# Performance work log

Hardware: AMD Instinct MI355X
Metric: run time of the kernel (lower is better)

The kernel has to match this reference:

```python
import jax, jax.numpy as jnp
import numpy as np

N, E, G = 50000, 400000, 64   # nodes, edges, graphs
HEADS = 4
F_IN, H1, C3, OUT = 64, 96, 64, 10  # in feats, hidden (3*32), last conv out, classes


def seg_softmax(alpha, index, num_segments):
    # numerically stable softmax over segments (PyG softmax(alpha, edge_index_i))
    amax = jax.ops.segment_max(alpha, index, num_segments)
    amax = jnp.where(jnp.isfinite(amax), amax, 0.0)
    e = jnp.exp(alpha - amax[index])
    denom = jax.ops.segment_sum(e, index, num_segments)
    return e / (denom[index] + 1e-16)


def general_conv(x, src, dst, Wm, bm, att, Ws=None, bs=None):
    # GeneralConv (attention=True, additive, directed_msg, aggr='add')
    C = att.shape[-1]
    m = (x[src] @ Wm + bm).reshape(-1, HEADS, C)              # [E,H,C] gathered messages
    a = jax.nn.leaky_relu((m * att).sum(-1), 0.2)             # [E,H] attention logits
    a = seg_softmax(a, dst, N)                                # segment softmax per dest node
    agg = jax.ops.segment_sum(m * a[..., None], dst, N)       # [N,H,C] scatter-add
    out = agg.mean(axis=1)                                    # head mean -> [N,C]
    if Ws is None:                                            # lin_self = Identity (in==out)
        return out + x
    return out + x @ Ws + bs


def setup_inputs():
    key = jax.random.key(0)
    ks = jax.random.split(key, 16)
    s = 0.05
    return {
        "x": jax.random.normal(ks[0], (N, F_IN), jnp.float32),
        "edge_index": jax.random.randint(ks[1], (2, E), 0, N, jnp.int32),
        "batch": jnp.sort(jax.random.randint(ks[2], (N,), 0, G, jnp.int32)),
        # layer 1: F_IN -> H1
        "Wm1": jax.random.normal(ks[3], (F_IN, HEADS * H1), jnp.float32) * s,
        "bm1": jnp.zeros((HEADS * H1,), jnp.float32),
        "att1": jax.random.normal(ks[4], (HEADS, H1), jnp.float32) * s,
        "Ws1": jax.random.normal(ks[5], (F_IN, H1), jnp.float32) * s,
        "bs1": jnp.zeros((H1,), jnp.float32),
        # layer 2: H1 -> H1 (lin_self = Identity)
        "Wm2": jax.random.normal(ks[6], (H1, HEADS * H1), jnp.float32) * s,
        "bm2": jnp.zeros((HEADS * H1,), jnp.float32),
        "att2": jax.random.normal(ks[7], (HEADS, H1), jnp.float32) * s,
        # layer 3: H1 -> C3
        "Wm3": jax.random.normal(ks[8], (H1, HEADS * C3), jnp.float32) * s,
        "bm3": jnp.zeros((HEADS * C3,), jnp.float32),
        "att3": jax.random.normal(ks[9], (HEADS, C3), jnp.float32) * s,
        "Ws3": jax.random.normal(ks[10], (H1, C3), jnp.float32) * s,
        "bs3": jnp.zeros((C3,), jnp.float32),
        # classifier
        "Wfc": jax.random.normal(ks[11], (C3, OUT), jnp.float32) * s,
        "bfc": jnp.zeros((OUT,), jnp.float32),
    }


def reference(x, edge_index, batch, Wm1, bm1, att1, Ws1, bs1,
              Wm2, bm2, att2, Wm3, bm3, att3, Ws3, bs3, Wfc, bfc):
    src, dst = edge_index[0], edge_index[1]
    h = general_conv(x, src, dst, Wm1, bm1, att1, Ws1, bs1)
    h = general_conv(h, src, dst, Wm2, bm2, att2)
    h = general_conv(h, src, dst, Wm3, bm3, att3, Ws3, bs3)
    # global_mean_pool
    ssum = jax.ops.segment_sum(h, batch, G)
    cnt = jax.ops.segment_sum(jnp.ones((N, 1), h.dtype), batch, G)
    pooled = ssum / jnp.maximum(cnt, 1.0)                      # [G,C3]
    logits = pooled @ Wfc + bfc
    return jax.nn.log_softmax(logits, axis=1)
```

## Files before the change

### kernel.cpp

```cpp
#include <hip/hip_runtime.h>
#include <hip/hip_bf16.h>
#include <stdint.h>

using bf16 = __hip_bfloat16;
typedef __attribute__((ext_vector_type(8))) short bf16x8;
typedef __attribute__((ext_vector_type(4))) float f32x4;
typedef __attribute__((ext_vector_type(2))) float f32x2;

#define NN 50000
#define NE 400000
#define NG 64
#define FIN 64
#define HID 96
#define CC3 64
#define NOUT 10

#define SCAN_BLOCK 256
#define NPART ((NN + SCAN_BLOCK - 1) / SCAN_BLOCK)

__device__ __forceinline__ float b2f(bf16 h){ return __bfloat162float(h); }
__device__ __forceinline__ bf16 f2b(float f){ return __float2bfloat16(f); }
__device__ __forceinline__ float blo(unsigned v){ return __uint_as_float(v << 16); }
__device__ __forceinline__ float bhi(unsigned v){ return __uint_as_float(v & 0xFFFF0000u); }

struct PrepA {
  const float *Wm1,*att1,*bm1,*Wm2,*att2,*bm2,*Wm3,*att3,*bm3,*bs1;
  float *f2,*f3,*lbv,*zb; bf16* WTf1;
  int* deg; float* psum; int* done;
};
__global__ __launch_bounds__(256) void prep_a_kernel(PrepA j){
  int bid = blockIdx.x;
  if (bid == 0){
    for (int i=threadIdx.x; i<96*4; i+=256){
      int k=i>>2, h=i&3; float a=0.f;
      for (int c=0;c<96;++c) a += j.Wm2[k*384 + h*96 + c]*j.att2[h*96+c];
      j.f2[i]=a;
    }
    for (int i=threadIdx.x; i<96*4; i+=256){
      int k=i>>2, h=i&3; float a=0.f;
      for (int c=0;c<64;++c) a += j.Wm3[k*256 + h*64 + c]*j.att3[h*64+c];
      j.f3[i]=a;
    }
    for (int i=threadIdx.x; i<16*64; i+=256){
      int col=i>>6, k=i&63; float a=0.f;
      if (col<4){ for (int c=0;c<96;++c) a += j.Wm1[k*384 + col*96 + c]*j.att1[col*96+c]; }
      j.WTf1[i] = f2b(a);
    }
    if (threadIdx.x < 96) j.zb[threadIdx.x] = 0.f;
    __syncthreads();
    if (threadIdx.x < 4){
      int h = threadIdx.x;
      float l1=0.f,l2=0.f,l3=0.f;
      for (int c=0;c<96;++c) l1 += j.bm1[h*96+c]*j.att1[h*96+c];
      for (int c=0;c<96;++c) l2 += j.bm2[h*96+c]*j.att2[h*96+c];
      for (int c=0;c<64;++c) l3 += j.bm3[h*64+c]*j.att3[h*64+c];
      float e2 = l2;
      for (int k=0;k<96;++k) e2 += j.bs1[k]*j.f2[k*4+h];
      j.lbv[h]=l1; j.lbv[4+h]=e2; j.lbv[8+h]=l3;
    }
  } else if (bid <= NPART){
    int i=(bid-1)*256+threadIdx.x;
    if (i<NN) j.deg[i]=0;
  } else {
    for (int i=threadIdx.x; i<NG*CC3; i+=256) j.psum[i]=0.f;
    if (threadIdx.x==0) *j.done = 0;
  }
}

struct PrepB {
  const float *Wm1,*bm1,*Ws1,*Wm2,*bm2,*Wm3,*bm3,*Ws3;
  const float *f2,*f3;
  bf16 *WT1,*WT2,*WT3;
};
__device__ __forceinline__ float w1full(const PrepB& j, int k, int c){
  if (k < 256) return 0.25f*j.Wm1[(k&63)*384 + (k>>6)*96 + c];
  if (k == 256) return 0.25f*(j.bm1[c]+j.bm1[96+c]+j.bm1[192+c]+j.bm1[288+c]);
  if (k < 288) return 0.f;
  return j.Ws1[(k-288)*96 + c];
}
__device__ __forceinline__ float w2full(const PrepB& j, int k, int c){
  if (k < 384){ int kk=k%96, h=k/96; return 0.25f*j.Wm2[kk*384 + h*96 + c]; }
  if (k == 384) return 0.25f*(j.bm2[c]+j.bm2[96+c]+j.bm2[192+c]+j.bm2[288+c]);
  if (k < 416) return 0.f;
  return (k-416==c) ? 1.f : 0.f;
}
__device__ __forceinline__ float w3full(const PrepB& j, int k, int c){
  if (k < 384){ int kk=k%96, h=k/96; return 0.25f*j.Wm3[kk*256 + h*64 + c]; }
  if (k == 384) return 0.25f*(j.bm3[c]+j.bm3[64+c]+j.bm3[128+c]+j.bm3[192+c]);
  if (k < 416) return 0.f;
  return j.Ws3[(k-416)*64 + c];
}
__global__ __launch_bounds__(256) void prep_b_kernel(PrepB j){
  int idx = blockIdx.x*256 + threadIdx.x;
  if (idx < 112*384){
    int col = idx/384, k = idx - col*384;
    float v;
    if (k >= 352) v = 0.f;
    else if (col < 96) v = w1full(j,k,col);
    else if (col < 100){ int h=col-96; float a=0.f;
      for (int c=0;c<96;++c) a += w1full(j,k,c)*j.f2[c*4+h]; v=a; }
    else v = 0.f;
    j.WT1[col*384 + k] = f2b(v);
  } else if (idx < 112*384 + 112*512){
    int r = idx - 112*384;
    int col = r/512, k = r - col*512;
    float v;
    if (col < 96) v = w2full(j,k,col);
    else if (col < 100){ int h=col-96; float a=0.f;
      for (int c=0;c<96;++c) a += w2full(j,k,c)*j.f3[c*4+h]; v=a; }
    else v = 0.f;
    j.WT2[col*512 + k] = f2b(v);
  } else {
    int r = idx - 112*384 - 112*512;
    int col = r/512, k = r - col*512;
    j.WT3[col*512 + k] = f2b(w3full(j,k,col));
  }
}

__global__ void deg_kernel(const int* __restrict__ ei, int* __restrict__ deg){
  int e = blockIdx.x*256 + threadIdx.x;
  if (e < NE) atomicAdd(&deg[ei[NE + e]], 1);
}

__global__ __launch_bounds__(256) void scan_part_kernel(const int* __restrict__ deg,
    int* __restrict__ partials, int* __restrict__ done, int* __restrict__ off){
  __shared__ int ws[4];
  __shared__ int lastflag;
  __shared__ int buf[256];
  int i = blockIdx.x*SCAN_BLOCK + threadIdx.x;
  int v = (i < NN) ? deg[i] : 0;
  int lane = threadIdx.x & 63, w = threadIdx.x >> 6;
  int s = v;
  #pragma unroll
  for (int m=1;m<64;m<<=1) s += __shfl_xor(s,m);
  if (lane==0) ws[w]=s;
  __syncthreads();
  if (threadIdx.x==0){
    int tot = ws[0]+ws[1]+ws[2]+ws[3];
    atomicExch(&partials[blockIdx.x], tot);
    __threadfence();
    int old = atomicAdd(done, 1);
    lastflag = (old == NPART-1) ? 1 : 0;
  }
  __syncthreads();
  if (lastflag){
    int t = threadIdx.x;
    int pv = (t < NPART) ? atomicAdd(&partials[t], 0) : 0;
    buf[t] = pv; __syncthreads();
    for (int st=1; st<256; st<<=1){
      int x = (t>=st) ? buf[t-st] : 0;
      __syncthreads();
      buf[t] += x;
      __syncthreads();
    }
    if (t < NPART) atomicExch(&partials[t], buf[t] - pv);
    if (t == 0) off[NN] = buf[255];
  }
}

__global__ __launch_bounds__(256) void scan_final_kernel(const int* __restrict__ deg,
    const int* __restrict__ partials, int* __restrict__ off, int* __restrict__ cursor){
  __shared__ int buf[256];
  int i = blockIdx.x*SCAN_BLOCK + threadIdx.x;
  int t = threadIdx.x;
  int v = (i<NN) ? deg[i] : 0;
  buf[t] = v; __syncthreads();
  for (int s=1;s<256;s<<=1){
    int x = (t>=s) ? buf[t-s] : 0;
    __syncthreads();
    buf[t] += x;
    __syncthreads();
  }
  int ex = partials[blockIdx.x] + buf[t] - v;
  if (i<NN){ off[i]=ex; cursor[i]=ex; }
}

__global__ void scatter_kernel(const int* __restrict__ ei, int* __restrict__ cursor,
                               int* __restrict__ csr_src){
  int e = blockIdx.x*256 + threadIdx.x;
  if (e < NE){
    int d = ei[NE + e];
    int slot = atomicAdd(&cursor[d], 1);
    csr_src[slot] = ei[e];
  }
}

__global__ __launch_bounds__(256) void el1_kernel(const float* __restrict__ x,
    const bf16* __restrict__ WTf1, const float* __restrict__ lbv,
    bf16* __restrict__ xb, uint8_t* __restrict__ x8, float* __restrict__ EL)
{
  const int wave = threadIdx.x>>6, lane = threadIdx.x&63;
  const int tile = blockIdx.x*4 + wave;
  if (tile >= NN/16) return;
  const int lm = lane&15, q = lane>>4;
  const size_t row = (size_t)tile*16 + lm;
  bf16x8 xf[2];
  #pragma unroll
  for (int kt=0;kt<2;++kt){
    float4 a0 = *(const float4*)(x + row*64 + kt*32 + q*8);
    float4 a1 = *(const float4*)(x + row*64 + kt*32 + q*8 + 4);
    bf16 t[8] = {f2b(a0.x),f2b(a0.y),f2b(a0.z),f2b(a0.w),
                 f2b(a1.x),f2b(a1.y),f2b(a1.z),f2b(a1.w)};
    xf[kt] = *(const bf16x8*)t;
    *(bf16x8*)(xb + row*64 + kt*32 + q*8) = xf[kt];
    int p0 = 0, p1 = 0;
    p0 = __builtin_amdgcn_cvt_pk_fp8_f32(a0.x, a0.y, p0, false);
    p0 = __builtin_amdgcn_cvt_pk_fp8_f32(a0.z, a0.w, p0, true);
    p1 = __builtin_amdgcn_cvt_pk_fp8_f32(a1.x, a1.y, p1, false);
    p1 = __builtin_amdgcn_cvt_pk_fp8_f32(a1.z, a1.w, p1, true);
    uint2 pk; pk.x = (unsigned)p0; pk.y = (unsigned)p1;
    *(uint2*)(x8 + row*64 + kt*32 + q*8) = pk;
  }
  f32x4 acc = {};
  #pragma unroll
  for (int kt=0;kt<2;++kt){
    bf16x8 wf = *(const bf16x8*)(WTf1 + (size_t)lm*64 + kt*32 + q*8);
    acc = __builtin_amdgcn_mfma_f32_16x16x32_bf16(wf, xf[kt], acc, 0,0,0);
  }
  if (q==0){
    float4 e; float l;
    l=acc[0]+lbv[0]; l=(l>=0.f)?l:0.2f*l; e.x=__expf(fminf(fmaxf(l,-60.f),60.f));
    l=acc[1]+lbv[1]; l=(l>=0.f)?l:0.2f*l; e.y=__expf(fminf(fmaxf(l,-60.f),60.f));
    l=acc[2]+lbv[2]; l=(l>=0.f)?l:0.2f*l; e.z=__expf(fminf(fmaxf(l,-60.f),60.f));
    l=acc[3]+lbv[3]; l=(l>=0.f)?l:0.2f*l; e.w=__expf(fminf(fmaxf(l,-60.f),60.f));
    *(float4*)(EL + 4*row) = e;
  }
}

template<int KH>
__global__ __launch_bounds__(256) void agg_kernel(
    const int* __restrict__ off, const int* __restrict__ csr_src,
    const float* __restrict__ ELin, const uint8_t* __restrict__ T8,
    bf16* __restrict__ Sb)
{
  constexpr int R  = 4*KH;
  constexpr int KS = R + 32;
  const int wave = threadIdx.x >> 6, lane = threadIdx.x & 63;
  const int n = blockIdx.x*4 + wave;
  const int e0 = off[n], e1 = off[n+1];

  const bool act = (8*lane) < R;
  const int hidx = min(3, (8*lane)/KH);
  const int kk = (8*lane) % KH;

  float acc[8] = {0.f,0.f,0.f,0.f,0.f,0.f,0.f,0.f};
  float dnl = 0.f;

  for (int base=e0; base<e1; base+=8){
    const int cnt = min(8, e1-base);
    int sreg = (lane < cnt) ? csr_src[base+lane] : 0;
    int sv[8];
    #pragma unroll
    for (int j=0;j<8;++j) sv[j] = __shfl(sreg, j);
    float wl[8]; uint2 u[8];
    #pragma unroll
    for (int j=0;j<8;++j){
      wl[j] = ELin[4*(size_t)sv[j] + hidx];
      u[j]  = *(const uint2*)(T8 + (size_t)sv[j]*KH + kk);
    }
    #pragma unroll
    for (int j=0;j<8;++j){
      float w = (j < cnt) ? wl[j] : 0.f;
      dnl += w;
      f32x2 a0 = __builtin_amdgcn_cvt_pk_f32_fp8((int)u[j].x, false);
      f32x2 a1 = __builtin_amdgcn_cvt_pk_f32_fp8((int)u[j].x, true);
      f32x2 a2 = __builtin_amdgcn_cvt_pk_f32_fp8((int)u[j].y, false);
      f32x2 a3 = __builtin_amdgcn_cvt_pk_f32_fp8((int)u[j].y, true);
      acc[0] += a0.x*w;  acc[1] += a0.y*w;
      acc[2] += a1.x*w;  acc[3] += a1.y*w;
      acc[4] += a2.x*w;  acc[5] += a2.y*w;
      acc[6] += a3.x*w;  acc[7] += a3.y*w;
    }
  }

  const float rd = 1.f/(dnl + 1e-16f);
  bf16* srow = Sb + (size_t)n*KS;
  if (act){
    bf16 st[8];
    #pragma unroll
    for (int t=0;t<8;++t) st[t] = f2b(acc[t]*rd);
    *(bf16x8*)(srow + 8*lane) = *(const bf16x8*)st;
  } else if (8*lane < KS){
    bf16 st[8] = {};
    if (8*lane == R) st[0] = f2b((e1 > e0) ? 1.f : 0.f);
    *(bf16x8*)(srow + 8*lane) = *(const bf16x8*)st;
  }
}

template<int KH, int NCT, bool POOL>
__global__ __launch_bounds__(256, 4) void gemm_kernel(
    const bf16* __restrict__ Sb, const bf16* __restrict__ Hprev,
    const bf16* __restrict__ WT, const float* __restrict__ bias,
    const float* __restrict__ lbe, bf16* __restrict__ Hout,
    uint8_t* __restrict__ H8out, float* __restrict__ ELout,
    const int* __restrict__ batch, float* __restrict__ psum)
{
  constexpr int R      = 4*KH;
  constexpr int KS     = R + 32;
  constexpr int KA     = KS + KH;
  constexpr int KTS    = KS/32;
  constexpr int NKT    = KA/32;
  constexpr int NCHUNK = (NKT + 3)/4;
  constexpr int KAP    = NCHUNK*128;
  constexpr int NCOL   = NCT*16;
  constexpr int NT     = NN/16;
  constexpr int WSZ    = NCOL*256;
  constexpr int OSZ    = POOL ? (4*16*68*4) : (4*16*104*2);
  constexpr int USZ    = (WSZ > OSZ) ? WSZ : OSZ;
  __shared__ __align__(16) unsigned char lds[USZ];

  const int tid  = threadIdx.x;
  const int wave = tid >> 6, lane = tid & 63;
  const int lm = lane & 15, q = lane >> 4;
  const int tile = blockIdx.x*4 + wave;
  const bool active = (tile < NT);
  const size_t row = (size_t)tile*16 + lm;

  const bf16* arow = Sb + row*KS;
  const bf16* hrow = Hprev + row*KH;
  const unsigned sw = (unsigned)((lm & 7) << 4);

  f32x4 acc[NCT];
  #pragma unroll
  for (int c=0;c<NCT;++c) acc[c] = (f32x4){0.f,0.f,0.f,0.f};

  #pragma unroll
  for (int chunk=0; chunk<NCHUNK; ++chunk){
    if (chunk) __syncthreads();
    {
      const int k0 = chunk*128;
      for (int idx = tid; idx < NCOL*16; idx += 256){
        const int col = idx >> 4, sg = idx & 15;
        uint4 v = *(const uint4*)(WT + (size_t)col*KAP + k0 + sg*8);
        const unsigned off = (unsigned)(sg*16) ^ (unsigned)((col & 7) << 4);
        *(uint4*)(lds + col*256 + off) = v;
      }
    }
    __syncthreads();
    if (active){
      bf16x8 a[4];
      #pragma unroll
      for (int t=0;t<4;++t){
        const int kt = chunk*4 + t;
        if (kt < KTS)      a[t] = *(const bf16x8*)(arow + kt*32 + q*8);
        else if (kt < NKT) a[t] = *(const bf16x8*)(hrow + (kt-KTS)*32 + q*8);
        else { bf16 z[8] = {}; a[t] = *(const bf16x8*)z; }
      }
      #pragma unroll
      for (int ct=0; ct<NCT; ++ct){
        const unsigned char* rbase = lds + (ct*16 + lm)*256;
        #pragma unroll
        for (int t=0;t<4;++t){
          bf16x8 wf = *(const bf16x8*)(rbase + (((unsigned)(t*64 + q*16)) ^ sw));
          acc[ct] = __builtin_amdgcn_mfma_f32_16x16x32_bf16(wf, a[t], acc[ct], 0,0,0);
        }
      }
    }
  }
  __syncthreads();

  if (active){
    if (!POOL){
      unsigned short* ob = (unsigned short*)(lds) + wave*16*104;
      #pragma unroll
      for (int ct=0; ct<NCT-1; ++ct){
        const int c = ct*16 + q*4;
        bf16 st[4] = {f2b(acc[ct][0]+bias[c]),   f2b(acc[ct][1]+bias[c+1]),
                      f2b(acc[ct][2]+bias[c+2]), f2b(acc[ct][3]+bias[c+3])};
        *(uint2*)(ob + lm*104 + c) = *(const uint2*)st;
      }
      if (q == 0){
        float4 e; float l;
        l=acc[NCT-1][0]+lbe[0]; l=(l>=0.f)?l:0.2f*l; e.x=__expf(fminf(fmaxf(l,-60.f),60.f));
        l=acc[NCT-1][1]+lbe[1]; l=(l>=0.f)?l:0.2f*l; e.y=__expf(fminf(fmaxf(l,-60.f),60.f));
        l=acc[NCT-1][2]+lbe[2]; l=(l>=0.f)?l:0.2f*l; e.z=__expf(fminf(fmaxf(l,-60.f),60.f));
        l=acc[NCT-1][3]+lbe[3]; l=(l>=0.f)?l:0.2f*l; e.w=__expf(fminf(fmaxf(l,-60.f),60.f));
        *(float4*)(ELout + 4*row) = e;
      }
      __builtin_amdgcn_wave_barrier();
      const size_t n0w = (size_t)tile*16;
      #pragma unroll
      for (int jj=0; jj<3; ++jj){
        const int idx = jj*64 + lane;
        const int r = idx/12, ch = idx - r*12;
        uint4 v = *(const uint4*)(ob + r*104 + ch*8);
        *(uint4*)(Hout + (n0w+r)*96 + ch*8) = v;
        int p0 = 0, p1 = 0;
        p0 = __builtin_amdgcn_cvt_pk_fp8_f32(blo(v.x), bhi(v.x), p0, false);
        p0 = __builtin_amdgcn_cvt_pk_fp8_f32(blo(v.y), bhi(v.y), p0, true);
        p1 = __builtin_amdgcn_cvt_pk_fp8_f32(blo(v.z), bhi(v.z), p1, false);
        p1 = __builtin_amdgcn_cvt_pk_fp8_f32(blo(v.w), bhi(v.w), p1, true);
        uint2 pk; pk.x = (unsigned)p0; pk.y = (unsigned)p1;
        *(uint2*)(H8out + (n0w+r)*96 + ch*8) = pk;
      }
    } else {
      float* ob = (float*)(lds) + wave*16*68;
      #pragma unroll
      for (int ct=0; ct<NCT; ++ct){
        const int c = ct*16 + q*4;
        float* orow = ob + lm*68;
        orow[c]   = acc[ct][0]+bias[c];   orow[c+1] = acc[ct][1]+bias[c+1];
        orow[c+2] = acc[ct][2]+bias[c+2]; orow[c+3] = acc[ct][3]+bias[c+3];
      }
      int bload = (lane < 16) ? batch[tile*16 + lane] : 0;
      __builtin_amdgcn_wave_barrier();
      const int c = lane;
      int curg = __shfl(bload, 0); float a = 0.f;
      #pragma unroll
      for (int i=0;i<16;++i){
        float v = ob[i*68 + c];
        int g = __shfl(bload, i);
        if (g != curg){ atomicAdd(&psum[curg*64+c], a); a=0.f; curg=g; }
        a += v;
      }
      atomicAdd(&psum[curg*64+c], a);
    }
  }
}

__global__ __launch_bounds__(64) void fc_kernel(const float* __restrict__ psum,
    const int* __restrict__ batch, const float* __restrict__ Wfc,
    const float* __restrict__ bfc, float* __restrict__ out){
  int g = blockIdx.x, t = threadIdx.x;
  __shared__ int sb[2];
  if (t < 2){
    int target = g + t;
    int lo=0, hi=NN;
    while (lo<hi){ int mid=(lo+hi)>>1; if (batch[mid]<target) lo=mid+1; else hi=mid; }
    sb[t]=lo;
  }
  __syncthreads();
  float cnt = (float)(sb[1]-sb[0]);
  __shared__ float p[CC3];
  __shared__ float lg[NOUT];
  p[t] = psum[g*CC3 + t] / fmaxf(cnt, 1.0f);
  __syncthreads();
  if (t < NOUT){
    float a = bfc[t];
    for (int c=0;c<CC3;++c) a += p[c]*Wfc[c*NOUT + t];
    lg[t] = a;
  }
  __syncthreads();
  if (t < NOUT){
    float m = -INFINITY;
    #pragma unroll
    for (int i=0;i<NOUT;++i) m = fmaxf(m, lg[i]);
    float s = 0.f;
    #pragma unroll
    for (int i=0;i<NOUT;++i) s += __expf(lg[i]-m);
    out[g*NOUT + t] = lg[t] - m - __logf(s);
  }
}

extern "C" void kernel_launch(void* const* d_in, const int* in_sizes, int n_in,
                              void* d_out, int out_size, void* d_ws, size_t ws_size,
                              hipStream_t stream) {
  const float* xf    = (const float*)d_in[0];
  const int*   ei    = (const int*)d_in[1];
  const int*   batch = (const int*)d_in[2];
  const float* pWm1  = (const float*)d_in[3];
  const float* pbm1  = (const float*)d_in[4];
  const float* patt1 = (const float*)d_in[5];
  const float* pWs1  = (const float*)d_in[6];
  const float* pbs1  = (const float*)d_in[7];
  const float* pWm2  = (const float*)d_in[8];
  const float* pbm2  = (const float*)d_in[9];
  const float* patt2 = (const float*)d_in[10];
  const float* pWm3  = (const float*)d_in[11];
  const float* pbm3  = (const float*)d_in[12];
  const float* patt3 = (const float*)d_in[13];
  const float* pWs3  = (const float*)d_in[14];
  const float* pbs3  = (const float*)d_in[15];
  const float* pWfc  = (const float*)d_in[16];
  const float* pbfc  = (const float*)d_in[17];

  char* p = (char*)d_ws;
  auto alloc = [&](size_t bytes)->char*{ char* q = p; p += (bytes + 255) & ~(size_t)255; return q; };
  int*     deg     = (int*)  alloc(NN*sizeof(int));
  int*     off     = (int*)  alloc((NN+1)*sizeof(int));
  int*     cursor  = (int*)  alloc(NN*sizeof(int));
  int*     csr_src = (int*)  alloc(NE*sizeof(int));
  int*     partials= (int*)  alloc(NPART*sizeof(int));
  int*     done    = (int*)  alloc(sizeof(int));
  float*   ELa     = (float*)alloc((size_t)NN*4*sizeof(float));
  float*   ELb     = (float*)alloc((size_t)NN*4*sizeof(float));
  bf16*    xb      = (bf16*) alloc((size_t)NN*64*sizeof(bf16));
  uint8_t* x8      = (uint8_t*)alloc((size_t)NN*64);
  uint8_t* H8      = (uint8_t*)alloc((size_t)NN*96);
  bf16*    H1b     = (bf16*) alloc((size_t)NN*96*sizeof(bf16));
  bf16*    H2b     = (bf16*) alloc((size_t)NN*96*sizeof(bf16));
  bf16*    Sb      = (bf16*) alloc((size_t)NN*416*sizeof(bf16));
  float*   psum    = (float*)alloc((size_t)NG*CC3*sizeof(float));
  float*   f2      = (float*)alloc(96*4*sizeof(float));
  float*   f3      = (float*)alloc(96*4*sizeof(float));
  float*   lbv     = (float*)alloc(12*sizeof(float));
  float*   zb      = (float*)alloc(96*sizeof(float));
  bf16*    WTf1    = (bf16*) alloc((size_t)16*64*sizeof(bf16));
  bf16*    WT1     = (bf16*) alloc((size_t)112*384*sizeof(bf16));
  bf16*    WT2     = (bf16*) alloc((size_t)112*512*sizeof(bf16));
  bf16*    WT3     = (bf16*) alloc((size_t)64*512*sizeof(bf16));

  PrepA pa;
  pa.Wm1=pWm1; pa.att1=patt1; pa.bm1=pbm1;
  pa.Wm2=pWm2; pa.att2=patt2; pa.bm2=pbm2;
  pa.Wm3=pWm3; pa.att3=patt3; pa.bm3=pbm3;
  pa.bs1=pbs1; pa.f2=f2; pa.f3=f3; pa.lbv=lbv; pa.zb=zb; pa.WTf1=WTf1;
  pa.deg=deg; pa.psum=psum; pa.done=done;
  prep_a_kernel<<<NPART+2, 256, 0, stream>>>(pa);

  PrepB pb;
  pb.Wm1=pWm1; pb.bm1=pbm1; pb.Ws1=pWs1;
  pb.Wm2=pWm2; pb.bm2=pbm2;
  pb.Wm3=pWm3; pb.bm3=pbm3; pb.Ws3=pWs3;
  pb.f2=f2; pb.f3=f3; pb.WT1=WT1; pb.WT2=WT2; pb.WT3=WT3;
  prep_b_kernel<<<(112*384 + 112*512 + 64*512)/256, 256, 0, stream>>>(pb);

  deg_kernel<<<(NE+255)/256, 256, 0, stream>>>(ei, deg);
  scan_part_kernel<<<NPART, 256, 0, stream>>>(deg, partials, done, off);
  scan_final_kernel<<<NPART, 256, 0, stream>>>(deg, partials, off, cursor);
  scatter_kernel<<<(NE+255)/256, 256, 0, stream>>>(ei, cursor, csr_src);

  el1_kernel<<<(NN/16+3)/4, 256, 0, stream>>>(xf, WTf1, lbv, xb, x8, ELa);

  const int AGB = NN/4;
  const int GGB = (NN/16 + 3)/4;

  agg_kernel<64><<<AGB, 256, 0, stream>>>(off, csr_src, ELa, x8, Sb);
  gemm_kernel<64,7,false><<<GGB, 256, 0, stream>>>(Sb, xb, WT1, pbs1, lbv+4,
                                                   H1b, H8, ELb, batch, psum);
  agg_kernel<96><<<AGB, 256, 0, stream>>>(off, csr_src, ELb, H8, Sb);
  gemm_kernel<96,7,false><<<GGB, 256, 0, stream>>>(Sb, H1b, WT2, zb, lbv+8,
                                                   H2b, H8, ELa, batch, psum);
  agg_kernel<96><<<AGB, 256, 0, stream>>>(off, csr_src, ELa, H8, Sb);
  gemm_kernel<96,4,true ><<<GGB, 256, 0, stream>>>(Sb, H2b, WT3, pbs3, nullptr,
                                                   nullptr, nullptr, nullptr, batch, psum);

  fc_kernel<<<NG, 64, 0, stream>>>(psum, batch, pWfc, pbfc, (float*)d_out);
}
```

Before: 340.9 us.

## Split GEMM column tiles across waves and use full-wave layout in layer-1 aggregation

The GEMM kernel now gives each block a single 16-row tile, with the four waves splitting the column tiles between them (two tiles per wave), instead of each wave computing every column tile for its own row tile. This launches four times as many blocks and lowers per-wave register and MFMA work, but it reloads the weight tile into LDS once per 16 rows and adds block-wide barriers in the epilogue. Separately, the KH=64 aggregation now has all 64 lanes load 4 fp8 bytes each, rather than 32 active lanes loading 8 bytes, which spreads the gather across the whole wave.

```diff
diff --git a/kernel.cpp b/kernel.cpp
--- a/kernel.cpp
+++ b/kernel.cpp
@@ -239,51 +239,86 @@
   const int n = blockIdx.x*4 + wave;
   const int e0 = off[n], e1 = off[n+1];
 
-  const bool act = (8*lane) < R;
-  const int hidx = min(3, (8*lane)/KH);
-  const int kk = (8*lane) % KH;
-
-  float acc[8] = {0.f,0.f,0.f,0.f,0.f,0.f,0.f,0.f};
-  float dnl = 0.f;
-
-  for (int base=e0; base<e1; base+=8){
-    const int cnt = min(8, e1-base);
-    int sreg = (lane < cnt) ? csr_src[base+lane] : 0;
-    int sv[8];
-    #pragma unroll
-    for (int j=0;j<8;++j) sv[j] = __shfl(sreg, j);
-    float wl[8]; uint2 u[8];
-    #pragma unroll
-    for (int j=0;j<8;++j){
-      wl[j] = ELin[4*(size_t)sv[j] + hidx];
-      u[j]  = *(const uint2*)(T8 + (size_t)sv[j]*KH + kk);
-    }
-    #pragma unroll
-    for (int j=0;j<8;++j){
-      float w = (j < cnt) ? wl[j] : 0.f;
-      dnl += w;
-      f32x2 a0 = __builtin_amdgcn_cvt_pk_f32_fp8((int)u[j].x, false);
-      f32x2 a1 = __builtin_amdgcn_cvt_pk_f32_fp8((int)u[j].x, true);
-      f32x2 a2 = __builtin_amdgcn_cvt_pk_f32_fp8((int)u[j].y, false);
-      f32x2 a3 = __builtin_amdgcn_cvt_pk_f32_fp8((int)u[j].y, true);
-      acc[0] += a0.x*w;  acc[1] += a0.y*w;
-      acc[2] += a1.x*w;  acc[3] += a1.y*w;
-      acc[4] += a2.x*w;  acc[5] += a2.y*w;
-      acc[6] += a3.x*w;  acc[7] += a3.y*w;
-    }
-  }
-
-  const float rd = 1.f/(dnl + 1e-16f);
-  bf16* srow = Sb + (size_t)n*KS;
-  if (act){
-    bf16 st[8];
-    #pragma unroll
-    for (int t=0;t<8;++t) st[t] = f2b(acc[t]*rd);
-    *(bf16x8*)(srow + 8*lane) = *(const bf16x8*)st;
-  } else if (8*lane < KS){
-    bf16 st[8] = {};
-    if (8*lane == R) st[0] = f2b((e1 > e0) ? 1.f : 0.f);
-    *(bf16x8*)(srow + 8*lane) = *(const bf16x8*)st;
+  if (KH == 64){
+    const int hidx = lane >> 4;
+    const int kk = (4*lane) & 63;
+    float acc[4] = {0.f,0.f,0.f,0.f};
+    float dnl = 0.f;
+    for (int base=e0; base<e1; base+=8){
+      const int cnt = min(8, e1-base);
+      int sreg = (lane < cnt) ? csr_src[base+lane] : 0;
+      int sv[8];
+      #pragma unroll
+      for (int j=0;j<8;++j) sv[j] = __shfl(sreg, j);
+      float wl[8]; unsigned u[8];
+      #pragma unroll
+      for (int j=0;j<8;++j){
+        wl[j] = ELin[4*(size_t)sv[j] + hidx];
+        u[j]  = *(const unsigned*)(T8 + (size_t)sv[j]*64 + kk);
+      }
+      #pragma unroll
+      for (int j=0;j<8;++j){
+        float w = (j < cnt) ? wl[j] : 0.f;
+        dnl += w;
+        f32x2 a0 = __builtin_amdgcn_cvt_pk_f32_fp8((int)u[j], false);
+        f32x2 a1 = __builtin_amdgcn_cvt_pk_f32_fp8((int)u[j], true);
+        acc[0] += a0.x*w;  acc[1] += a0.y*w;
+        acc[2] += a1.x*w;  acc[3] += a1.y*w;
+      }
+    }
+    const float rd = 1.f/(dnl + 1e-16f);
+    bf16* srow = Sb + (size_t)n*KS;
+    bf16 st[4] = {f2b(acc[0]*rd), f2b(acc[1]*rd), f2b(acc[2]*rd), f2b(acc[3]*rd)};
+    *(uint2*)(srow + hidx*64 + kk) = *(const uint2*)st;
+    if (lane < 8){
+      uint2 z; z.x = 0u; z.y = 0u;
+      if (lane == 0 && e1 > e0) z.x = 0x3F80u;
+      *(uint2*)(srow + R + lane*4) = z;
+    }
+  } else {
+    const bool act = (8*lane) < R;
+    const int hidx = min(3, (8*lane)/KH);
+    const int kk = (8*lane) % KH;
+    float acc[8] = {0.f,0.f,0.f,0.f,0.f,0.f,0.f,0.f};
+    float dnl = 0.f;
+    for (int base=e0; base<e1; base+=8){
+      const int cnt = min(8, e1-base);
+      int sreg = (lane < cnt) ? csr_src[base+lane] : 0;
+      int sv[8];
+      #pragma unroll
+      for (int j=0;j<8;++j) sv[j] = __shfl(sreg, j);
+      float wl[8]; uint2 u[8];
+      #pragma unroll
+      for (int j=0;j<8;++j){
+        wl[j] = ELin[4*(size_t)sv[j] + hidx];
+        u[j]  = *(const uint2*)(T8 + (size_t)sv[j]*KH + kk);
+      }
+      #pragma unroll
+      for (int j=0;j<8;++j){
+        float w = (j < cnt) ? wl[j] : 0.f;
+        dnl += w;
+        f32x2 a0 = __builtin_amdgcn_cvt_pk_f32_fp8((int)u[j].x, false);
+        f32x2 a1 = __builtin_amdgcn_cvt_pk_f32_fp8((int)u[j].x, true);
+        f32x2 a2 = __builtin_amdgcn_cvt_pk_f32_fp8((int)u[j].y, false);
+        f32x2 a3 = __builtin_amdgcn_cvt_pk_f32_fp8((int)u[j].y, true);
+        acc[0] += a0.x*w;  acc[1] += a0.y*w;
+        acc[2] += a1.x*w;  acc[3] += a1.y*w;
+        acc[4] += a2.x*w;  acc[5] += a2.y*w;
+        acc[6] += a3.x*w;  acc[7] += a3.y*w;
+      }
+    }
+    const float rd = 1.f/(dnl + 1e-16f);
+    bf16* srow = Sb + (size_t)n*KS;
+    if (act){
+      bf16 st[8];
+      #pragma unroll
+      for (int t=0;t<8;++t) st[t] = f2b(acc[t]*rd);
+      *(bf16x8*)(srow + 8*lane) = *(const bf16x8*)st;
+    } else if (8*lane < KS){
+      bf16 st[8] = {};
+      if (8*lane == R) st[0] = f2b((e1 > e0) ? 1.f : 0.f);
+      *(bf16x8*)(srow + 8*lane) = *(const bf16x8*)st;
+    }
   }
 }
 
@@ -303,33 +338,36 @@
   constexpr int NCHUNK = (NKT + 3)/4;
   constexpr int KAP    = NCHUNK*128;
   constexpr int NCOL   = NCT*16;
-  constexpr int NT     = NN/16;
   constexpr int WSZ    = NCOL*256;
-  constexpr int OSZ    = POOL ? (4*16*68*4) : (4*16*104*2);
+  constexpr int OSZ    = POOL ? (16*68*4) : (16*104*2);
   constexpr int USZ    = (WSZ > OSZ) ? WSZ : OSZ;
   __shared__ __align__(16) unsigned char lds[USZ];
+  __shared__ int sbat[16];
 
   const int tid  = threadIdx.x;
   const int wave = tid >> 6, lane = tid & 63;
   const int lm = lane & 15, q = lane >> 4;
-  const int tile = blockIdx.x*4 + wave;
-  const bool active = (tile < NT);
+  const int tile = blockIdx.x;
   const size_t row = (size_t)tile*16 + lm;
+
+  if (POOL && tid < 16) sbat[tid] = batch[tile*16 + tid];
 
   const bf16* arow = Sb + row*KS;
   const bf16* hrow = Hprev + row*KH;
   const unsigned sw = (unsigned)((lm & 7) << 4);
 
-  f32x4 acc[NCT];
-  #pragma unroll
-  for (int c=0;c<NCT;++c) acc[c] = (f32x4){0.f,0.f,0.f,0.f};
+  f32x4 acc0 = {0.f,0.f,0.f,0.f};
+  f32x4 acc1 = {0.f,0.f,0.f,0.f};
+  const int ct0 = wave, ct1 = wave + 4;
 
   #pragma unroll
   for (int chunk=0; chunk<NCHUNK; ++chunk){
     if (chunk) __syncthreads();
     {
       const int k0 = chunk*128;
-      for (int idx = tid; idx < NCOL*16; idx += 256){
+      #pragma unroll
+      for (int it=0; it<NCOL*16/256; ++it){
+        const int idx = it*256 + tid;
         const int col = idx >> 4, sg = idx & 15;
         uint4 v = *(const uint4*)(WT + (size_t)col*KAP + k0 + sg*8);
         const unsigned off = (unsigned)(sg*16) ^ (unsigned)((col & 7) << 4);
@@ -337,79 +375,86 @@
       }
     }
     __syncthreads();
-    if (active){
-      bf16x8 a[4];
+    bf16x8 a[4];
+    #pragma unroll
+    for (int t=0;t<4;++t){
+      const int kt = chunk*4 + t;
+      if (kt < KTS)      a[t] = *(const bf16x8*)(arow + kt*32 + q*8);
+      else if (kt < NKT) a[t] = *(const bf16x8*)(hrow + (kt-KTS)*32 + q*8);
+      else { bf16 z[8] = {}; a[t] = *(const bf16x8*)z; }
+    }
+    {
+      const unsigned char* rbase = lds + (ct0*16 + lm)*256;
       #pragma unroll
       for (int t=0;t<4;++t){
-        const int kt = chunk*4 + t;
-        if (kt < KTS)      a[t] = *(const bf16x8*)(arow + kt*32 + q*8);
-        else if (kt < NKT) a[t] = *(const bf16x8*)(hrow + (kt-KTS)*32 + q*8);
-        else { bf16 z[8] = {}; a[t] = *(const bf16x8*)z; }
-      }
-      #pragma unroll
-      for (int ct=0; ct<NCT; ++ct){
-        const unsigned char* rbase = lds + (ct*16 + lm)*256;
-        #pragma unroll
-        for (int t=0;t<4;++t){
-          bf16x8 wf = *(const bf16x8*)(rbase + (((unsigned)(t*64 + q*16)) ^ sw));
-          acc[ct] = __builtin_amdgcn_mfma_f32_16x16x32_bf16(wf, a[t], acc[ct], 0,0,0);
+        bf16x8 wf = *(const bf16x8*)(rbase + (((unsigned)(t*64 + q*16)) ^ sw));
+        acc0 = __builtin_amdgcn_mfma_f32_16x16x32_bf16(wf, a[t], acc0, 0,0,0);
+      }
+    }
+    if (ct1 < NCT){
+      const unsigned char* rbase = lds + (ct1*16 + lm)*256;
+      #pragma unroll
+      for (int t=0;t<4;++t){
+        bf16x8 wf = *(const bf16x8*)(rbase + (((unsigned)(t*64 + q*16)) ^ sw));
+        acc1 = __builtin_amdgcn_mfma_f32_16x16x32_bf16(wf, a[t], acc1, 0,0,0);
+      }
+    }
+  }
+  __syncthreads();
+
+  if (!POOL){
+    unsigned short* ob = (unsigned short*)lds;
+    #pragma unroll
+    for (int k=0;k<2;++k){
+      const int ct = k ? ct1 : ct0;
+      if (ct >= NCT) continue;
+      const f32x4 v = k ? acc1 : acc0;
+      if (ct == NCT-1){
+        if (q == 0){
+          float4 e; float l;
+          l=v[0]+lbe[0]; l=(l>=0.f)?l:0.2f*l; e.x=__expf(fminf(fmaxf(l,-60.f),60.f));
+          l=v[1]+lbe[1]; l=(l>=0.f)?l:0.2f*l; e.y=__expf(fminf(fmaxf(l,-60.f),60.f));
+          l=v[2]+lbe[2]; l=(l>=0.f)?l:0.2f*l; e.z=__expf(fminf(fmaxf(l,-60.f),60.f));
+          l=v[3]+lbe[3]; l=(l>=0.f)?l:0.2f*l; e.w=__expf(fminf(fmaxf(l,-60.f),60.f));
+          *(float4*)(ELout + 4*row) = e;
         }
-      }
-    }
-  }
-  __syncthreads();
-
-  if (active){
-    if (!POOL){
-      unsigned short* ob = (unsigned short*)(lds) + wave*16*104;
-      #pragma unroll
-      for (int ct=0; ct<NCT-1; ++ct){
+      } else {
         const int c = ct*16 + q*4;
-        bf16 st[4] = {f2b(acc[ct][0]+bias[c]),   f2b(acc[ct][1]+bias[c+1]),
-                      f2b(acc[ct][2]+bias[c+2]), f2b(acc[ct][3]+bias[c+3])};
+        bf16 st[4] = {f2b(v[0]+bias[c]),   f2b(v[1]+bias[c+1]),
+                      f2b(v[2]+bias[c+2]), f2b(v[3]+bias[c+3])};
         *(uint2*)(ob + lm*104 + c) = *(const uint2*)st;
       }
-      if (q == 0){
-        float4 e; float l;
-        l=acc[NCT-1][0]+lbe[0]; l=(l>=0.f)?l:0.2f*l; e.x=__expf(fminf(fmaxf(l,-60.f),60.f));
-        l=acc[NCT-1][1]+lbe[1]; l=(l>=0.f)?l:0.2f*l; e.y=__expf(fminf(fmaxf(l,-60.f),60.f));
-        l=acc[NCT-1][2]+lbe[2]; l=(l>=0.f)?l:0.2f*l; e.z=__expf(fminf(fmaxf(l,-60.f),60.f));
-        l=acc[NCT-1][3]+lbe[3]; l=(l>=0.f)?l:0.2f*l; e.w=__expf(fminf(fmaxf(l,-60.f),60.f));
-        *(float4*)(ELout + 4*row) = e;
-      }
-      __builtin_amdgcn_wave_barrier();
+    }
+    __syncthreads();
+    if (tid < 192){
+      const int r = tid/12, ch = tid - r*12;
       const size_t n0w = (size_t)tile*16;
-      #pragma unroll
-      for (int jj=0; jj<3; ++jj){
-        const int idx = jj*64 + lane;
-        const int r = idx/12, ch = idx - r*12;
-        uint4 v = *(const uint4*)(ob + r*104 + ch*8);
-        *(uint4*)(Hout + (n0w+r)*96 + ch*8) = v;
-        int p0 = 0, p1 = 0;
-        p0 = __builtin_amdgcn_cvt_pk_fp8_f32(blo(v.x), bhi(v.x), p0, false);
-        p0 = __builtin_amdgcn_cvt_pk_fp8_f32(blo(v.y), bhi(v.y), p0, true);
-        p1 = __builtin_amdgcn_cvt_pk_fp8_f32(blo(v.z), bhi(v.z), p1, false);
-        p1 = __builtin_amdgcn_cvt_pk_fp8_f32(blo(v.w), bhi(v.w), p1, true);
-        uint2 pk; pk.x = (unsigned)p0; pk.y = (unsigned)p1;
-        *(uint2*)(H8out + (n0w+r)*96 + ch*8) = pk;
-      }
-    } else {
-      float* ob = (float*)(lds) + wave*16*68;
-      #pragma unroll
-      for (int ct=0; ct<NCT; ++ct){
-        const int c = ct*16 + q*4;
-        float* orow = ob + lm*68;
-        orow[c]   = acc[ct][0]+bias[c];   orow[c+1] = acc[ct][1]+bias[c+1];
-        orow[c+2] = acc[ct][2]+bias[c+2]; orow[c+3] = acc[ct][3]+bias[c+3];
-      }
-      int bload = (lane < 16) ? batch[tile*16 + lane] : 0;
-      __builtin_amdgcn_wave_barrier();
-      const int c = lane;
-      int curg = __shfl(bload, 0); float a = 0.f;
+      uint4 v = *(const uint4*)(ob + r*104 + ch*8);
+      *(uint4*)(Hout + (n0w+r)*96 + ch*8) = v;
+      int p0 = 0, p1 = 0;
+      p0 = __builtin_amdgcn_cvt_pk_fp8_f32(blo(v.x), bhi(v.x), p0, false);
+      p0 = __builtin_amdgcn_cvt_pk_fp8_f32(blo(v.y), bhi(v.y), p0, true);
+      p1 = __builtin_amdgcn_cvt_pk_fp8_f32(blo(v.z), bhi(v.z), p1, false);
+      p1 = __builtin_amdgcn_cvt_pk_fp8_f32(blo(v.w), bhi(v.w), p1, true);
+      uint2 pk; pk.x = (unsigned)p0; pk.y = (unsigned)p1;
+      *(uint2*)(H8out + (n0w+r)*96 + ch*8) = pk;
+    }
+  } else {
+    float* ob = (float*)lds;
+    {
+      const int c = ct0*16 + q*4;
+      float* orow = ob + lm*68;
+      orow[c]   = acc0[0]+bias[c];   orow[c+1] = acc0[1]+bias[c+1];
+      orow[c+2] = acc0[2]+bias[c+2]; orow[c+3] = acc0[3]+bias[c+3];
+    }
+    __syncthreads();
+    if (tid < 64){
+      const int c = tid;
+      int curg = sbat[0]; float a = 0.f;
       #pragma unroll
       for (int i=0;i<16;++i){
         float v = ob[i*68 + c];
-        int g = __shfl(bload, i);
+        int g = sbat[i];
         if (g != curg){ atomicAdd(&psum[curg*64+c], a); a=0.f; curg=g; }
         a += v;
       }
@@ -523,7 +568,7 @@
   el1_kernel<<<(NN/16+3)/4, 256, 0, stream>>>(xf, WTf1, lbv, xb, x8, ELa);
 
   const int AGB = NN/4;
-  const int GGB = (NN/16 + 3)/4;
+  const int GGB = NN/16;
 
   agg_kernel<64><<<AGB, 256, 0, stream>>>(off, csr_src, ELa, x8, Sb);
   gemm_kernel<64,7,false><<<GGB, 256, 0, stream>>>(Sb, xb, WT1, pbs1, lbv+4,
```

After: 354.1 us. +3.9%, slower.
